# Performance work log

Measured on AMD Instinct MI355X. Metric: run time of the kernel, lower is better.

Reference implementation:

```python
import jax, jax.numpy as jnp
import numpy as np

C = 256
NH = 8
G = 32  # groupnorm groups (min(32, C))
EPS = 1e-6


def setup_inputs() -> dict:
    key = jax.random.key(0)
    ks = jax.random.split(key, 7)
    B, D, H, W = 2, 16, 16, 16
    x = jax.random.normal(ks[0], (B, C, D, H, W), dtype=jnp.float32)
    gn_gamma = jnp.ones((C,), jnp.float32)
    gn_beta = jnp.zeros((C,), jnp.float32)
    s = 1.0 / np.sqrt(C)
    qkv_w = jax.random.normal(ks[1], (3 * C, C), jnp.float32) * s  # 1x1x1 conv weight
    qkv_b = jnp.zeros((3 * C,), jnp.float32)
    proj_w = jax.random.normal(ks[2], (C, C), jnp.float32) * s
    proj_b = jnp.zeros((C,), jnp.float32)
    return {"x": x, "gn_gamma": gn_gamma, "gn_beta": gn_beta,
            "qkv_w": qkv_w, "qkv_b": qkv_b, "proj_w": proj_w, "proj_b": proj_b}


def _group_norm(x, gamma, beta):
    # x: [B, C, S]
    B, Cc, S = x.shape
    xg = x.reshape(B, G, (Cc // G) * S)
    mu = xg.mean(axis=-1, keepdims=True)
    var = xg.var(axis=-1, keepdims=True)
    xg = (xg - mu) * jax.lax.rsqrt(var + EPS)
    x = xg.reshape(B, Cc, S)
    return x * gamma[None, :, None] + beta[None, :, None]


def reference(x, gn_gamma, gn_beta, qkv_w, qkv_b, proj_w, proj_b):
    B, Cc, D, H, W = x.shape
    S = D * H * W
    hd = Cc // NH
    xf = x.reshape(B, Cc, S)
    h = _group_norm(xf, gn_gamma, gn_beta)
    # 1x1x1 conv == channel matmul: [B, 3C, S]
    qkv = jnp.einsum('oc,bcs->bos', qkv_w, h) + qkv_b[None, :, None]
    # torch path: reshape(B,3C,S).permute(0,2,1).chunk -> q=channels[0:C]
    q, k, v = qkv[:, :Cc], qkv[:, Cc:2 * Cc], qkv[:, 2 * Cc:]
    # [B, C, S] -> [B, NH, S, hd]
    def to_heads(t):
        return t.reshape(B, NH, hd, S).transpose(0, 1, 3, 2)
    q, k, v = to_heads(q), to_heads(k), to_heads(v)
    scale = hd ** (-0.5)
    attn = jax.nn.softmax(jnp.einsum('bnqd,bnkd->bnqk', q, k) * scale, axis=-1)
    o = jnp.einsum('bnqk,bnkd->bnqd', attn, v)  # [B, NH, S, hd]
    o = o.transpose(0, 1, 3, 2).reshape(B, Cc, S)  # back to [B, C, S]
    o = jnp.einsum('oc,bcs->bos', proj_w, o) + proj_b[None, :, None]
    return x + o.reshape(B, Cc, D, H, W)
```

## Files before the change

kernel.cpp:

```cpp
#include <hip/hip_runtime.h>
#include <cstddef>

#define S_LEN 4096
#define C_DIM 256
#define NHEADS 8
#define HDIM 32

typedef __attribute__((ext_vector_type(8))) _Float16 half8;
typedef __attribute__((ext_vector_type(4))) _Float16 half4;
typedef __attribute__((ext_vector_type(2))) _Float16 h2t;
typedef __attribute__((ext_vector_type(2))) __fp16 fp16x2;
typedef __attribute__((ext_vector_type(4))) float floatx4;

#define SC2F ((float)(0.17677669529663687 * 1.4426950408889634))

__global__ __launch_bounds__(256) void prep_stats(
    const float* __restrict__ qkv_w, const float* __restrict__ proj_w,
    const float* __restrict__ qkv_b, const float* __restrict__ x,
    _Float16* __restrict__ wq, _Float16* __restrict__ wp,
    float* __restrict__ qbias, float* __restrict__ gstat)
{
  const int blk = blockIdx.x;
  const int tid = threadIdx.x;
  if (blk < 64) {
    __shared__ float red[2][4];
    const int g = blk & 31, b = blk >> 5;
    const float* xb = x + ((size_t)b * C_DIM + g * 8) * S_LEN;
    const float4* x4 = (const float4*)xb;
    float sum = 0.f, sumsq = 0.f;
    for (int i = tid; i < 8192; i += 256) {
      float4 v = x4[i];
      sum += v.x + v.y + v.z + v.w;
      sumsq += v.x * v.x + v.y * v.y + v.z * v.z + v.w * v.w;
    }
    for (int off = 1; off < 64; off <<= 1) {
      sum += __shfl_xor(sum, off, 64);
      sumsq += __shfl_xor(sumsq, off, 64);
    }
    const int wv = tid >> 6, lane = tid & 63;
    if (lane == 0) { red[0][wv] = sum; red[1][wv] = sumsq; }
    __syncthreads();
    if (tid == 0) {
      float s = red[0][0] + red[0][1] + red[0][2] + red[0][3];
      float sq = red[1][0] + red[1][1] + red[1][2] + red[1][3];
      float mean = s * (1.f / 32768.f);
      float var = sq * (1.f / 32768.f) - mean * mean;
      gstat[((size_t)b * 32 + g) * 2 + 0] = mean;
      gstat[((size_t)b * 32 + g) * 2 + 1] = rsqrtf(var + 1e-6f);
    }
  } else {
    int idx = (blk - 64) * 256 + tid;
    if (idx < 768 * 256) {
      float v = qkv_w[idx];
      if (idx < 256 * 256) v *= SC2F;
      wq[idx] = (_Float16)v;
    } else if (idx < 768 * 256 + 256 * 256) {
      int i = idx - 768 * 256;
      wp[i] = (_Float16)proj_w[i];
    } else if (idx < 768 * 256 + 256 * 256 + 768) {
      int i = idx - (768 * 256 + 256 * 256);
      float bv = qkv_b[i];
      if (i < 256) bv *= SC2F;
      qbias[i] = bv;
    }
  }
}

__global__ __launch_bounds__(256) void qkv_gn_gemm(
    const _Float16* __restrict__ W, const float* __restrict__ bias,
    const float* __restrict__ x, const float* __restrict__ gamma,
    const float* __restrict__ beta, const float* __restrict__ gstat,
    _Float16* __restrict__ qo, _Float16* __restrict__ ko_,
    _Float16* __restrict__ vo)
{
  __shared__ __align__(16) _Float16 Ld[64 * 264];
  const int tid = threadIdx.x;
  const int b = blockIdx.z;
  const int s0 = blockIdx.y * 64;

  {
    const int c0 = (tid & 127) * 2, c1 = c0 + 1;
    const int sh = tid >> 7;
    const int g = c0 >> 3;
    const float mean = gstat[((size_t)b * 32 + g) * 2 + 0];
    const float rstd = gstat[((size_t)b * 32 + g) * 2 + 1];
    const float ga0 = gamma[c0] * rstd, be0 = beta[c0] - mean * ga0;
    const float ga1 = gamma[c1] * rstd, be1 = beta[c1] - mean * ga1;
    const float4* xa = (const float4*)(x + ((size_t)b * C_DIM + c0) * S_LEN + s0 + sh * 32);
    const float4* xc = (const float4*)(x + ((size_t)b * C_DIM + c1) * S_LEN + s0 + sh * 32);
    #pragma unroll
    for (int j = 0; j < 8; ++j) {
      float4 a = xa[j], c = xc[j];
      int sl = sh * 32 + j * 4;
      *(h2t*)&Ld[(sl + 0) * 264 + c0] = (h2t){ (_Float16)(a.x * ga0 + be0), (_Float16)(c.x * ga1 + be1) };
      *(h2t*)&Ld[(sl + 1) * 264 + c0] = (h2t){ (_Float16)(a.y * ga0 + be0), (_Float16)(c.y * ga1 + be1) };
      *(h2t*)&Ld[(sl + 2) * 264 + c0] = (h2t){ (_Float16)(a.z * ga0 + be0), (_Float16)(c.z * ga1 + be1) };
      *(h2t*)&Ld[(sl + 3) * 264 + c0] = (h2t){ (_Float16)(a.w * ga0 + be0), (_Float16)(c.w * ga1 + be1) };
    }
  }
  __syncthreads();

  const int lane = tid & 63, wv = tid >> 6;
  const int m = lane & 15, quad = lane >> 4;
  const int mtb = blockIdx.x * 8 + wv * 2;
  const _Float16* wrow0 = W + (size_t)((mtb + 0) * 16 + m) * C_DIM + quad * 8;
  const _Float16* wrow1 = W + (size_t)((mtb + 1) * 16 + m) * C_DIM + quad * 8;
  const _Float16* lp = &Ld[m * 264 + quad * 8];

  floatx4 acc[2][4];
  #pragma unroll
  for (int j = 0; j < 2; ++j)
    #pragma unroll
    for (int s = 0; s < 4; ++s) acc[j][s] = (floatx4){0.f,0.f,0.f,0.f};

  #pragma unroll
  for (int k0 = 0; k0 < C_DIM; k0 += 32) {
    half8 b0 = *(const half8*)(lp + k0);
    half8 b1 = *(const half8*)(lp + 16 * 264 + k0);
    half8 b2 = *(const half8*)(lp + 32 * 264 + k0);
    half8 b3 = *(const half8*)(lp + 48 * 264 + k0);
    half8 a0 = *(const half8*)(wrow0 + k0);
    half8 a1 = *(const half8*)(wrow1 + k0);
    acc[0][0] = __builtin_amdgcn_mfma_f32_16x16x32_f16(a0, b0, acc[0][0], 0, 0, 0);
    acc[0][1] = __builtin_amdgcn_mfma_f32_16x16x32_f16(a0, b1, acc[0][1], 0, 0, 0);
    acc[0][2] = __builtin_amdgcn_mfma_f32_16x16x32_f16(a0, b2, acc[0][2], 0, 0, 0);
    acc[0][3] = __builtin_amdgcn_mfma_f32_16x16x32_f16(a0, b3, acc[0][3], 0, 0, 0);
    acc[1][0] = __builtin_amdgcn_mfma_f32_16x16x32_f16(a1, b0, acc[1][0], 0, 0, 0);
    acc[1][1] = __builtin_amdgcn_mfma_f32_16x16x32_f16(a1, b1, acc[1][1], 0, 0, 0);
    acc[1][2] = __builtin_amdgcn_mfma_f32_16x16x32_f16(a1, b2, acc[1][2], 0, 0, 0);
    acc[1][3] = __builtin_amdgcn_mfma_f32_16x16x32_f16(a1, b3, acc[1][3], 0, 0, 0);
  }

  #pragma unroll
  for (int j = 0; j < 2; ++j) {
    const int ob = (mtb + j) * 16 + quad * 4;
    const float bv0 = bias[ob], bv1 = bias[ob + 1],
                bv2 = bias[ob + 2], bv3 = bias[ob + 3];
    #pragma unroll
    for (int sub = 0; sub < 4; ++sub) {
      int s = s0 + sub * 16 + m;
      float v0 = acc[j][sub][0] + bv0, v1 = acc[j][sub][1] + bv1,
            v2 = acc[j][sub][2] + bv2, v3 = acc[j][sub][3] + bv3;
      if (ob < 512) {
        _Float16* dst = (ob < 256) ? qo : ko_;
        int oo = ob & 255, n = oo >> 5, d0 = oo & 31;
        half4 h = { (_Float16)v0, (_Float16)v1, (_Float16)v2, (_Float16)v3 };
        *(half4*)(dst + (((size_t)b * NHEADS + n) * S_LEN + s) * HDIM + d0) = h;
      } else {
        int oo = ob - 512, n = oo >> 5, d0 = oo & 31;
        _Float16* dst = vo + ((size_t)b * NHEADS + n) * HDIM * S_LEN + s;
        dst[(size_t)(d0 + 0) * S_LEN] = (_Float16)v0;
        dst[(size_t)(d0 + 1) * S_LEN] = (_Float16)v1;
        dst[(size_t)(d0 + 2) * S_LEN] = (_Float16)v2;
        dst[(size_t)(d0 + 3) * S_LEN] = (_Float16)v3;
      }
    }
  }
}

__global__ __launch_bounds__(512) void attn_kernel(
    const _Float16* __restrict__ q, const _Float16* __restrict__ k,
    const _Float16* __restrict__ v, _Float16* __restrict__ po,
    float* __restrict__ pl)
{
  __shared__ __align__(16) _Float16 Kl[2][128 * 40];
  __shared__ __align__(16) _Float16 Vl[2][32 * 136];
  const int tid = threadIdx.x;
  const int lane = tid & 63, wv = tid >> 6;
  const int m = lane & 15, quad = lane >> 4;
  const int n = blockIdx.y, b = blockIdx.z;
  const int qc = blockIdx.x >> 1, kh = blockIdx.x & 1;
  const int q0 = qc * 128 + wv * 16;
  const int bh = b * NHEADS + n;

  const _Float16* qb = q + (size_t)bh * S_LEN * HDIM;
  const _Float16* kb = k + (size_t)bh * S_LEN * HDIM + (size_t)kh * 2048 * HDIM;
  const _Float16* vb = v + (size_t)bh * HDIM * S_LEN + (size_t)kh * 2048;

  half8 qf = *(const half8*)(qb + (size_t)(q0 + m) * HDIM + quad * 8);

  const int krow = tid >> 2, kc = (tid & 3) * 8;
  const int vrow = tid >> 4, vc = (tid & 15) * 8;
  const _Float16* kg = kb + (size_t)krow * HDIM + kc;
  const _Float16* vg = vb + (size_t)vrow * S_LEN + vc;
  const int klds = krow * 40 + kc;
  const int vlds = vrow * 136 + vc;

  int4 kreg = *(const int4*)kg;
  int4 vreg = *(const int4*)vg;
  const _Float16* kgp = kg + 128 * HDIM;
  const _Float16* vgp = vg + 128;

  floatx4 o0 = {0.f,0.f,0.f,0.f}, o1 = o0;
  float l0 = 0.f;
  const fp16x2 one2 = { (__fp16)1.0f, (__fp16)1.0f };

  #pragma unroll 2
  for (int it = 0; it < 16; ++it) {
    const int bufi = it & 1;
    *(int4*)(&Kl[bufi][klds]) = kreg;
    *(int4*)(&Vl[bufi][vlds]) = vreg;
    kreg = *(const int4*)kgp; kgp += 128 * HDIM;
    vreg = *(const int4*)vgp; vgp += 128;
    __syncthreads();
    const _Float16* Kb = Kl[bufi];
    const _Float16* Vb = Vl[bufi];
    #pragma unroll
    for (int t = 0; t < 8; ++t) {
      half8 kf = *(const half8*)(Kb + (t * 16 + m) * 40 + quad * 8);
      half4 vf0 = *(const half4*)(Vb + m * 136 + t * 16 + quad * 4);
      half4 vf1 = *(const half4*)(Vb + (16 + m) * 136 + t * 16 + quad * 4);
      floatx4 z = {0.f,0.f,0.f,0.f};
      floatx4 s0 = __builtin_amdgcn_mfma_f32_16x16x32_f16(kf, qf, z, 0, 0, 0);
      float e0 = __builtin_amdgcn_exp2f(s0[0]);
      float e1 = __builtin_amdgcn_exp2f(s0[1]);
      float e2 = __builtin_amdgcn_exp2f(s0[2]);
      float e3 = __builtin_amdgcn_exp2f(s0[3]);
      half4 p0;
      fp16x2 plo = __builtin_amdgcn_cvt_pkrtz(e0, e1);
      fp16x2 phi = __builtin_amdgcn_cvt_pkrtz(e2, e3);
      *(fp16x2*)&p0 = plo;
      *((fp16x2*)&p0 + 1) = phi;
      l0 = __builtin_amdgcn_fdot2(plo, one2, l0, false);
      l0 = __builtin_amdgcn_fdot2(phi, one2, l0, false);
      o0 = __builtin_amdgcn_mfma_f32_16x16x16f16(vf0, p0, o0, 0, 0, 0);
      o1 = __builtin_amdgcn_mfma_f32_16x16x16f16(vf1, p0, o1, 0, 0, 0);
    }
  }
  l0 += __shfl_xor(l0, 16, 64);
  l0 += __shfl_xor(l0, 32, 64);
  _Float16* poh = po + (size_t)kh * 2097152 + ((size_t)bh * S_LEN + q0 + m) * HDIM;
  half4 h0 = { (_Float16)o0[0], (_Float16)o0[1], (_Float16)o0[2], (_Float16)o0[3] };
  half4 h1 = { (_Float16)o1[0], (_Float16)o1[1], (_Float16)o1[2], (_Float16)o1[3] };
  *(half4*)(poh + quad * 4) = h0;
  *(half4*)(poh + 16 + quad * 4) = h1;
  if (quad == 0) pl[(size_t)kh * 65536 + (size_t)bh * S_LEN + q0 + m] = l0;
}

__global__ __launch_bounds__(256) void proj_gemm(
    const _Float16* __restrict__ W, const float* __restrict__ bias,
    const _Float16* __restrict__ po, const float* __restrict__ pl,
    const float* __restrict__ x, float* __restrict__ out)
{
  const int tid = threadIdx.x;
  const int lane = tid & 63, wv = tid >> 6;
  const int m = lane & 15, quad = lane >> 4;
  const int mt = blockIdx.x * 4 + wv;
  const int s0 = blockIdx.y * 64;
  const int b = blockIdx.z;
  const int row = mt * 16 + m;

  float inv[8][4];
  #pragma unroll
  for (int n = 0; n < 8; ++n) {
    #pragma unroll
    for (int sub = 0; sub < 4; ++sub) {
      size_t idx = ((size_t)(b * NHEADS + n)) * S_LEN + s0 + sub * 16 + m;
      inv[n][sub] = 1.f / (pl[idx] + pl[65536 + idx]);
    }
  }

  const _Float16* wrow = W + (size_t)row * C_DIM + quad * 8;
  floatx4 acc0 = {0.f,0.f,0.f,0.f}, acc1 = acc0, acc2 = acc0, acc3 = acc0;
  #pragma unroll
  for (int k0 = 0; k0 < C_DIM; k0 += 32) {
    const int n = k0 >> 5;
    const int d0 = quad * 8;
    half8 bf[4];
    #pragma unroll
    for (int sub = 0; sub < 4; ++sub) {
      size_t idx = (((size_t)(b * NHEADS + n)) * S_LEN + s0 + sub * 16 + m) * HDIM + d0;
      half8 a = *(const half8*)(po + idx);
      half8 c = *(const half8*)(po + 2097152 + idx);
      _Float16 iv = (_Float16)inv[n][sub];
      bf[sub] = (a + c) * iv;
    }
    half8 af = *(const half8*)(wrow + k0);
    acc0 = __builtin_amdgcn_mfma_f32_16x16x32_f16(af, bf[0], acc0, 0, 0, 0);
    acc1 = __builtin_amdgcn_mfma_f32_16x16x32_f16(af, bf[1], acc1, 0, 0, 0);
    acc2 = __builtin_amdgcn_mfma_f32_16x16x32_f16(af, bf[2], acc2, 0, 0, 0);
    acc3 = __builtin_amdgcn_mfma_f32_16x16x32_f16(af, bf[3], acc3, 0, 0, 0);
  }
  floatx4 accs[4] = {acc0, acc1, acc2, acc3};
  #pragma unroll
  for (int sub = 0; sub < 4; ++sub) {
    int s = s0 + sub * 16 + m;
    #pragma unroll
    for (int r = 0; r < 4; ++r) {
      int c = mt * 16 + quad * 4 + r;
      size_t idx = ((size_t)b * C_DIM + c) * S_LEN + s;
      out[idx] = x[idx] + accs[sub][r] + bias[c];
    }
  }
}

extern "C" void kernel_launch(void* const* d_in, const int* in_sizes, int n_in,
                              void* d_out, int out_size, void* d_ws, size_t ws_size,
                              hipStream_t stream) {
  const float* x        = (const float*)d_in[0];
  const float* gn_gamma = (const float*)d_in[1];
  const float* gn_beta  = (const float*)d_in[2];
  const float* qkv_w    = (const float*)d_in[3];
  const float* qkv_b    = (const float*)d_in[4];
  const float* proj_w   = (const float*)d_in[5];
  const float* proj_b   = (const float*)d_in[6];
  float* out = (float*)d_out;

  const size_t n1 = (size_t)2 * S_LEN * C_DIM;
  char* ws = (char*)d_ws;
  _Float16* qx  = (_Float16*)ws;
  _Float16* kx  = qx + n1;
  _Float16* vx  = kx + n1;
  _Float16* wq  = vx + n1;
  _Float16* wp  = wq + 768 * 256;
  float*    qbias = (float*)(wp + 256 * 256);
  float*    gstat = qbias + 768;
  _Float16* po  = (_Float16*)(gstat + 128);
  float*    pl  = (float*)(po + 2 * n1);

  prep_stats<<<1091, 256, 0, stream>>>(qkv_w, proj_w, qkv_b, x, wq, wp, qbias, gstat);
  qkv_gn_gemm<<<dim3(6, 64, 2), 256, 0, stream>>>(wq, qbias, x, gn_gamma, gn_beta, gstat, qx, kx, vx);
  attn_kernel<<<dim3(64, 8, 2), 512, 0, stream>>>(qx, kx, vx, po, pl);
  proj_gemm<<<dim3(4, 64, 2), 256, 0, stream>>>(wp, proj_b, po, pl, x, out);
}
```

Measured before the change: 171.1 us.

## Split keys across waves in attention, keep all queries in registers

Restructures the attention kernel so each of 4 waves holds all 128 query rows in registers and processes its own 32-key slice of each 128-key chunk. K and V fragments are loaded directly from global memory into registers, with no LDS staging and no per-iteration barrier. Partial outputs and row sums from the waves are reduced through LDS in a two-step tree at the end. This removes the LDS round-trip and the synchronization in the main loop, but greatly raises register pressure (16 accumulators plus 8 Q fragments) and halves the threads per block, which can lower occupancy. It also rounds the partial sums to fp16 during the cross-wave reduction.

```diff
diff --git a/kernel.cpp b/kernel.cpp
--- a/kernel.cpp
+++ b/kernel.cpp
@@ -158,83 +158,146 @@
   }
 }
 
-__global__ __launch_bounds__(512) void attn_kernel(
+__global__ __launch_bounds__(256) void attn_kernel(
     const _Float16* __restrict__ q, const _Float16* __restrict__ k,
     const _Float16* __restrict__ v, _Float16* __restrict__ po,
     float* __restrict__ pl)
 {
-  __shared__ __align__(16) _Float16 Kl[2][128 * 40];
-  __shared__ __align__(16) _Float16 Vl[2][32 * 136];
+  __shared__ unsigned int Ml[2][64][41];
   const int tid = threadIdx.x;
   const int lane = tid & 63, wv = tid >> 6;
   const int m = lane & 15, quad = lane >> 4;
   const int n = blockIdx.y, b = blockIdx.z;
   const int qc = blockIdx.x >> 1, kh = blockIdx.x & 1;
-  const int q0 = qc * 128 + wv * 16;
+  const int q0 = qc * 128;
   const int bh = b * NHEADS + n;
 
   const _Float16* qb = q + (size_t)bh * S_LEN * HDIM;
   const _Float16* kb = k + (size_t)bh * S_LEN * HDIM + (size_t)kh * 2048 * HDIM;
   const _Float16* vb = v + (size_t)bh * HDIM * S_LEN + (size_t)kh * 2048;
 
-  half8 qf = *(const half8*)(qb + (size_t)(q0 + m) * HDIM + quad * 8);
-
-  const int krow = tid >> 2, kc = (tid & 3) * 8;
-  const int vrow = tid >> 4, vc = (tid & 15) * 8;
-  const _Float16* kg = kb + (size_t)krow * HDIM + kc;
-  const _Float16* vg = vb + (size_t)vrow * S_LEN + vc;
-  const int klds = krow * 40 + kc;
-  const int vlds = vrow * 136 + vc;
-
-  int4 kreg = *(const int4*)kg;
-  int4 vreg = *(const int4*)vg;
-  const _Float16* kgp = kg + 128 * HDIM;
-  const _Float16* vgp = vg + 128;
-
-  floatx4 o0 = {0.f,0.f,0.f,0.f}, o1 = o0;
-  float l0 = 0.f;
+  half8 qf[8];
+  #pragma unroll
+  for (int j = 0; j < 8; ++j)
+    qf[j] = *(const half8*)(qb + (size_t)(q0 + j * 16 + m) * HDIM + quad * 8);
+
+  const _Float16* kp0 = kb + (size_t)(wv * 32 + m) * HDIM + quad * 8;
+  const _Float16* kp1 = kp0 + 16 * HDIM;
+  const _Float16* vp00 = vb + (size_t)m * S_LEN + wv * 32 + quad * 4;
+  const _Float16* vp01 = vp00 + 16;
+  const _Float16* vp10 = vp00 + (size_t)16 * S_LEN;
+  const _Float16* vp11 = vp10 + 16;
+
+  int4 kr0 = *(const int4*)kp0, kr1 = *(const int4*)kp1;
+  int2 v00 = *(const int2*)vp00, v01 = *(const int2*)vp01;
+  int2 v10 = *(const int2*)vp10, v11 = *(const int2*)vp11;
+
+  floatx4 o[8][2];
+  float l[8];
+  #pragma unroll
+  for (int j = 0; j < 8; ++j) {
+    o[j][0] = (floatx4){0.f,0.f,0.f,0.f};
+    o[j][1] = (floatx4){0.f,0.f,0.f,0.f};
+    l[j] = 0.f;
+  }
   const fp16x2 one2 = { (__fp16)1.0f, (__fp16)1.0f };
 
-  #pragma unroll 2
   for (int it = 0; it < 16; ++it) {
-    const int bufi = it & 1;
-    *(int4*)(&Kl[bufi][klds]) = kreg;
-    *(int4*)(&Vl[bufi][vlds]) = vreg;
-    kreg = *(const int4*)kgp; kgp += 128 * HDIM;
-    vreg = *(const int4*)vgp; vgp += 128;
-    __syncthreads();
-    const _Float16* Kb = Kl[bufi];
-    const _Float16* Vb = Vl[bufi];
-    #pragma unroll
-    for (int t = 0; t < 8; ++t) {
-      half8 kf = *(const half8*)(Kb + (t * 16 + m) * 40 + quad * 8);
-      half4 vf0 = *(const half4*)(Vb + m * 136 + t * 16 + quad * 4);
-      half4 vf1 = *(const half4*)(Vb + (16 + m) * 136 + t * 16 + quad * 4);
+    half8 kf0 = __builtin_bit_cast(half8, kr0);
+    half8 kf1 = __builtin_bit_cast(half8, kr1);
+    half4 vf00 = __builtin_bit_cast(half4, v00);
+    half4 vf01 = __builtin_bit_cast(half4, v01);
+    half4 vf10 = __builtin_bit_cast(half4, v10);
+    half4 vf11 = __builtin_bit_cast(half4, v11);
+    kp0 += 128 * HDIM; kp1 += 128 * HDIM;
+    vp00 += 128; vp01 += 128; vp10 += 128; vp11 += 128;
+    kr0 = *(const int4*)kp0; kr1 = *(const int4*)kp1;
+    v00 = *(const int2*)vp00; v01 = *(const int2*)vp01;
+    v10 = *(const int2*)vp10; v11 = *(const int2*)vp11;
+    #pragma unroll
+    for (int j = 0; j < 8; ++j) {
       floatx4 z = {0.f,0.f,0.f,0.f};
-      floatx4 s0 = __builtin_amdgcn_mfma_f32_16x16x32_f16(kf, qf, z, 0, 0, 0);
+      floatx4 s0 = __builtin_amdgcn_mfma_f32_16x16x32_f16(kf0, qf[j], z, 0, 0, 0);
+      floatx4 s1 = __builtin_amdgcn_mfma_f32_16x16x32_f16(kf1, qf[j], z, 0, 0, 0);
       float e0 = __builtin_amdgcn_exp2f(s0[0]);
       float e1 = __builtin_amdgcn_exp2f(s0[1]);
       float e2 = __builtin_amdgcn_exp2f(s0[2]);
       float e3 = __builtin_amdgcn_exp2f(s0[3]);
-      half4 p0;
-      fp16x2 plo = __builtin_amdgcn_cvt_pkrtz(e0, e1);
-      fp16x2 phi = __builtin_amdgcn_cvt_pkrtz(e2, e3);
-      *(fp16x2*)&p0 = plo;
-      *((fp16x2*)&p0 + 1) = phi;
-      l0 = __builtin_amdgcn_fdot2(plo, one2, l0, false);
-      l0 = __builtin_amdgcn_fdot2(phi, one2, l0, false);
-      o0 = __builtin_amdgcn_mfma_f32_16x16x16f16(vf0, p0, o0, 0, 0, 0);
-      o1 = __builtin_amdgcn_mfma_f32_16x16x16f16(vf1, p0, o1, 0, 0, 0);
-    }
-  }
-  l0 += __shfl_xor(l0, 16, 64);
-  l0 += __shfl_xor(l0, 32, 64);
-  _Float16* poh = po + (size_t)kh * 2097152 + ((size_t)bh * S_LEN + q0 + m) * HDIM;
-  half4 h0 = { (_Float16)o0[0], (_Float16)o0[1], (_Float16)o0[2], (_Float16)o0[3] };
-  half4 h1 = { (_Float16)o1[0], (_Float16)o1[1], (_Float16)o1[2], (_Float16)o1[3] };
-  *(half4*)(poh + quad * 4) = h0;
-  *(half4*)(poh + 16 + quad * 4) = h1;
-  if (quad == 0) pl[(size_t)kh * 65536 + (size_t)bh * S_LEN + q0 + m] = l0;
+      float f0 = __builtin_amdgcn_exp2f(s1[0]);
+      float f1 = __builtin_amdgcn_exp2f(s1[1]);
+      float f2 = __builtin_amdgcn_exp2f(s1[2]);
+      float f3 = __builtin_amdgcn_exp2f(s1[3]);
+      half4 p0, p1;
+      fp16x2 p0lo = __builtin_amdgcn_cvt_pkrtz(e0, e1);
+      fp16x2 p0hi = __builtin_amdgcn_cvt_pkrtz(e2, e3);
+      fp16x2 p1lo = __builtin_amdgcn_cvt_pkrtz(f0, f1);
+      fp16x2 p1hi = __builtin_amdgcn_cvt_pkrtz(f2, f3);
+      *(fp16x2*)&p0 = p0lo; *((fp16x2*)&p0 + 1) = p0hi;
+      *(fp16x2*)&p1 = p1lo; *((fp16x2*)&p1 + 1) = p1hi;
+      float lj = l[j];
+      lj = __builtin_amdgcn_fdot2(p0lo, one2, lj, false);
+      lj = __builtin_amdgcn_fdot2(p0hi, one2, lj, false);
+      lj = __builtin_amdgcn_fdot2(p1lo, one2, lj, false);
+      lj = __builtin_amdgcn_fdot2(p1hi, one2, lj, false);
+      l[j] = lj;
+      o[j][0] = __builtin_amdgcn_mfma_f32_16x16x16f16(vf00, p0, o[j][0], 0, 0, 0);
+      o[j][1] = __builtin_amdgcn_mfma_f32_16x16x16f16(vf10, p0, o[j][1], 0, 0, 0);
+      o[j][0] = __builtin_amdgcn_mfma_f32_16x16x16f16(vf01, p1, o[j][0], 0, 0, 0);
+      o[j][1] = __builtin_amdgcn_mfma_f32_16x16x16f16(vf11, p1, o[j][1], 0, 0, 0);
+    }
+  }
+
+  #define WRITE_SLOT(s)                                                      \
+    { unsigned int* d_ = &Ml[s][lane][0];                                    \
+      _Pragma("unroll") for (int j = 0; j < 8; ++j) {                        \
+        half4 h0_ = { (_Float16)o[j][0][0], (_Float16)o[j][0][1],            \
+                      (_Float16)o[j][0][2], (_Float16)o[j][0][3] };          \
+        half4 h1_ = { (_Float16)o[j][1][0], (_Float16)o[j][1][1],            \
+                      (_Float16)o[j][1][2], (_Float16)o[j][1][3] };          \
+        int2 a_ = __builtin_bit_cast(int2, h0_);                             \
+        int2 b_ = __builtin_bit_cast(int2, h1_);                             \
+        d_[j*4+0] = a_.x; d_[j*4+1] = a_.y;                                  \
+        d_[j*4+2] = b_.x; d_[j*4+3] = b_.y; }                                \
+      _Pragma("unroll") for (int j = 0; j < 8; ++j)                          \
+        d_[32+j] = __builtin_bit_cast(unsigned int, l[j]); }
+  #define ADD_SLOT(s)                                                        \
+    { const unsigned int* r_ = &Ml[s][lane][0];                              \
+      _Pragma("unroll") for (int j = 0; j < 8; ++j) {                        \
+        int2 a_ = { (int)r_[j*4+0], (int)r_[j*4+1] };                        \
+        int2 b_ = { (int)r_[j*4+2], (int)r_[j*4+3] };                        \
+        half4 h0_ = __builtin_bit_cast(half4, a_);                           \
+        half4 h1_ = __builtin_bit_cast(half4, b_);                           \
+        _Pragma("unroll") for (int r2 = 0; r2 < 4; ++r2) {                   \
+          o[j][0][r2] += (float)h0_[r2];                                     \
+          o[j][1][r2] += (float)h1_[r2]; } }                                 \
+      _Pragma("unroll") for (int j = 0; j < 8; ++j)                          \
+        l[j] += __builtin_bit_cast(float, r_[32+j]); }
+
+  if (wv >= 2) WRITE_SLOT(wv - 2);
+  __syncthreads();
+  if (wv < 2) ADD_SLOT(wv);
+  __syncthreads();
+  if (wv == 1) WRITE_SLOT(0);
+  __syncthreads();
+  if (wv == 0) {
+    ADD_SLOT(0);
+    _Float16* pob = po + (size_t)kh * 2097152 + ((size_t)bh * S_LEN) * HDIM;
+    #pragma unroll
+    for (int j = 0; j < 8; ++j) {
+      float lj = l[j];
+      lj += __shfl_xor(lj, 16, 64);
+      lj += __shfl_xor(lj, 32, 64);
+      int qrow = q0 + j * 16 + m;
+      half4 h0 = { (_Float16)o[j][0][0], (_Float16)o[j][0][1],
+                   (_Float16)o[j][0][2], (_Float16)o[j][0][3] };
+      half4 h1 = { (_Float16)o[j][1][0], (_Float16)o[j][1][1],
+                   (_Float16)o[j][1][2], (_Float16)o[j][1][3] };
+      _Float16* poh = pob + (size_t)qrow * HDIM;
+      *(half4*)(poh + quad * 4) = h0;
+      *(half4*)(poh + 16 + quad * 4) = h1;
+      if (quad == 0) pl[(size_t)kh * 65536 + (size_t)bh * S_LEN + qrow] = lj;
+    }
+  }
 }
 
 __global__ __launch_bounds__(256) void proj_gemm(
@@ -320,6 +383,6 @@
 
   prep_stats<<<1091, 256, 0, stream>>>(qkv_w, proj_w, qkv_b, x, wq, wp, qbias, gstat);
   qkv_gn_gemm<<<dim3(6, 64, 2), 256, 0, stream>>>(wq, qbias, x, gn_gamma, gn_beta, gstat, qx, kx, vx);
-  attn_kernel<<<dim3(64, 8, 2), 512, 0, stream>>>(qx, kx, vx, po, pl);
+  attn_kernel<<<dim3(64, 8, 2), 256, 0, stream>>>(qx, kx, vx, po, pl);
   proj_gemm<<<dim3(4, 64, 2), 256, 0, stream>>>(wp, proj_b, po, pl, x, out);
 }
```

New measurement: 191.4 us. 1.12x slower.

## Split groupnorm stats across more blocks and shrink attention K/V tiles

Applied to the files above, without the earlier changes.

The group-norm statistics pass is spread over 512 blocks that each write partial sums and sums of squares. The consuming GEMM kernel then reduces the 8 partials per group to get mean and rstd. This is meant to replace 64 long serial blocks with a wider, more parallel reduction. Separately, the attention kernel's K/V staging tile is halved from 128 to 64 keys, doubling loop iterations with smaller LDS buffers and 8-byte loads. That adds more barriers per key range in exchange for lower LDS use.

```diff
diff --git a/kernel.cpp b/kernel.cpp
--- a/kernel.cpp
+++ b/kernel.cpp
@@ -18,18 +18,20 @@
     const float* __restrict__ qkv_w, const float* __restrict__ proj_w,
     const float* __restrict__ qkv_b, const float* __restrict__ x,
     _Float16* __restrict__ wq, _Float16* __restrict__ wp,
-    float* __restrict__ qbias, float* __restrict__ gstat)
+    float* __restrict__ qbias, float* __restrict__ pstat)
 {
   const int blk = blockIdx.x;
   const int tid = threadIdx.x;
-  if (blk < 64) {
+  if (blk < 512) {
     __shared__ float red[2][4];
-    const int g = blk & 31, b = blk >> 5;
-    const float* xb = x + ((size_t)b * C_DIM + g * 8) * S_LEN;
+    const int gb = blk >> 3, e = blk & 7;
+    const int g = gb & 31, b = gb >> 5;
+    const float* xb = x + ((size_t)b * C_DIM + g * 8) * S_LEN + e * 4096;
     const float4* x4 = (const float4*)xb;
     float sum = 0.f, sumsq = 0.f;
-    for (int i = tid; i < 8192; i += 256) {
-      float4 v = x4[i];
+    #pragma unroll
+    for (int i = 0; i < 4; ++i) {
+      float4 v = x4[tid + i * 256];
       sum += v.x + v.y + v.z + v.w;
       sumsq += v.x * v.x + v.y * v.y + v.z * v.z + v.w * v.w;
     }
@@ -41,15 +43,11 @@
     if (lane == 0) { red[0][wv] = sum; red[1][wv] = sumsq; }
     __syncthreads();
     if (tid == 0) {
-      float s = red[0][0] + red[0][1] + red[0][2] + red[0][3];
-      float sq = red[1][0] + red[1][1] + red[1][2] + red[1][3];
-      float mean = s * (1.f / 32768.f);
-      float var = sq * (1.f / 32768.f) - mean * mean;
-      gstat[((size_t)b * 32 + g) * 2 + 0] = mean;
-      gstat[((size_t)b * 32 + g) * 2 + 1] = rsqrtf(var + 1e-6f);
+      pstat[(gb * 8 + e) * 2 + 0] = red[0][0] + red[0][1] + red[0][2] + red[0][3];
+      pstat[(gb * 8 + e) * 2 + 1] = red[1][0] + red[1][1] + red[1][2] + red[1][3];
     }
   } else {
-    int idx = (blk - 64) * 256 + tid;
+    int idx = (blk - 512) * 256 + tid;
     if (idx < 768 * 256) {
       float v = qkv_w[idx];
       if (idx < 256 * 256) v *= SC2F;
@@ -69,7 +67,7 @@
 __global__ __launch_bounds__(256) void qkv_gn_gemm(
     const _Float16* __restrict__ W, const float* __restrict__ bias,
     const float* __restrict__ x, const float* __restrict__ gamma,
-    const float* __restrict__ beta, const float* __restrict__ gstat,
+    const float* __restrict__ beta, const float* __restrict__ pstat,
     _Float16* __restrict__ qo, _Float16* __restrict__ ko_,
     _Float16* __restrict__ vo)
 {
@@ -82,8 +80,15 @@
     const int c0 = (tid & 127) * 2, c1 = c0 + 1;
     const int sh = tid >> 7;
     const int g = c0 >> 3;
-    const float mean = gstat[((size_t)b * 32 + g) * 2 + 0];
-    const float rstd = gstat[((size_t)b * 32 + g) * 2 + 1];
+    const int gb = b * 32 + g;
+    float s = 0.f, sq = 0.f;
+    #pragma unroll
+    for (int e = 0; e < 8; ++e) {
+      s  += pstat[(gb * 8 + e) * 2 + 0];
+      sq += pstat[(gb * 8 + e) * 2 + 1];
+    }
+    const float mean = s * (1.f / 32768.f);
+    const float rstd = rsqrtf(sq * (1.f / 32768.f) - mean * mean + 1e-6f);
     const float ga0 = gamma[c0] * rstd, be0 = beta[c0] - mean * ga0;
     const float ga1 = gamma[c1] * rstd, be1 = beta[c1] - mean * ga1;
     const float4* xa = (const float4*)(x + ((size_t)b * C_DIM + c0) * S_LEN + s0 + sh * 32);
@@ -163,8 +168,8 @@
     const _Float16* __restrict__ v, _Float16* __restrict__ po,
     float* __restrict__ pl)
 {
-  __shared__ __align__(16) _Float16 Kl[2][128 * 40];
-  __shared__ __align__(16) _Float16 Vl[2][32 * 136];
+  __shared__ __align__(16) _Float16 Kl[2][64 * 40];
+  __shared__ __align__(16) _Float16 Vl[2][32 * 68];
   const int tid = threadIdx.x;
   const int lane = tid & 63, wv = tid >> 6;
   const int m = lane & 15, quad = lane >> 4;
@@ -179,37 +184,37 @@
 
   half8 qf = *(const half8*)(qb + (size_t)(q0 + m) * HDIM + quad * 8);
 
-  const int krow = tid >> 2, kc = (tid & 3) * 8;
-  const int vrow = tid >> 4, vc = (tid & 15) * 8;
+  const int krow = wv * 8 + (lane >> 3), kc = (lane & 7) * 4;
+  const int vrow = wv * 4 + (lane >> 4), vc = (lane & 15) * 4;
   const _Float16* kg = kb + (size_t)krow * HDIM + kc;
   const _Float16* vg = vb + (size_t)vrow * S_LEN + vc;
   const int klds = krow * 40 + kc;
-  const int vlds = vrow * 136 + vc;
-
-  int4 kreg = *(const int4*)kg;
-  int4 vreg = *(const int4*)vg;
-  const _Float16* kgp = kg + 128 * HDIM;
-  const _Float16* vgp = vg + 128;
+  const int vlds = vrow * 68 + vc;
+
+  int2 kreg = *(const int2*)kg;
+  int2 vreg = *(const int2*)vg;
+  const _Float16* kgp = kg + 64 * HDIM;
+  const _Float16* vgp = vg + 64;
 
   floatx4 o0 = {0.f,0.f,0.f,0.f}, o1 = o0;
   float l0 = 0.f;
   const fp16x2 one2 = { (__fp16)1.0f, (__fp16)1.0f };
 
   #pragma unroll 2
-  for (int it = 0; it < 16; ++it) {
+  for (int it = 0; it < 32; ++it) {
     const int bufi = it & 1;
-    *(int4*)(&Kl[bufi][klds]) = kreg;
-    *(int4*)(&Vl[bufi][vlds]) = vreg;
-    kreg = *(const int4*)kgp; kgp += 128 * HDIM;
-    vreg = *(const int4*)vgp; vgp += 128;
+    *(int2*)(&Kl[bufi][klds]) = kreg;
+    *(int2*)(&Vl[bufi][vlds]) = vreg;
+    kreg = *(const int2*)kgp; kgp += 64 * HDIM;
+    vreg = *(const int2*)vgp; vgp += 64;
     __syncthreads();
     const _Float16* Kb = Kl[bufi];
     const _Float16* Vb = Vl[bufi];
     #pragma unroll
-    for (int t = 0; t < 8; ++t) {
+    for (int t = 0; t < 4; ++t) {
       half8 kf = *(const half8*)(Kb + (t * 16 + m) * 40 + quad * 8);
-      half4 vf0 = *(const half4*)(Vb + m * 136 + t * 16 + quad * 4);
-      half4 vf1 = *(const half4*)(Vb + (16 + m) * 136 + t * 16 + quad * 4);
+      half4 vf0 = *(const half4*)(Vb + m * 68 + t * 16 + quad * 4);
+      half4 vf1 = *(const half4*)(Vb + (16 + m) * 68 + t * 16 + quad * 4);
       floatx4 z = {0.f,0.f,0.f,0.f};
       floatx4 s0 = __builtin_amdgcn_mfma_f32_16x16x32_f16(kf, qf, z, 0, 0, 0);
       float e0 = __builtin_amdgcn_exp2f(s0[0]);
@@ -314,12 +319,12 @@
   _Float16* wq  = vx + n1;
   _Float16* wp  = wq + 768 * 256;
   float*    qbias = (float*)(wp + 256 * 256);
-  float*    gstat = qbias + 768;
-  _Float16* po  = (_Float16*)(gstat + 128);
+  float*    pstat = qbias + 768;
+  _Float16* po  = (_Float16*)(pstat + 1024);
   float*    pl  = (float*)(po + 2 * n1);
 
-  prep_stats<<<1091, 256, 0, stream>>>(qkv_w, proj_w, qkv_b, x, wq, wp, qbias, gstat);
-  qkv_gn_gemm<<<dim3(6, 64, 2), 256, 0, stream>>>(wq, qbias, x, gn_gamma, gn_beta, gstat, qx, kx, vx);
+  prep_stats<<<1539, 256, 0, stream>>>(qkv_w, proj_w, qkv_b, x, wq, wp, qbias, pstat);
+  qkv_gn_gemm<<<dim3(6, 64, 2), 256, 0, stream>>>(wq, qbias, x, gn_gamma, gn_beta, pstat, qx, kx, vx);
   attn_kernel<<<dim3(64, 8, 2), 512, 0, stream>>>(qx, kx, vx, po, pl);
   proj_gemm<<<dim3(4, 64, 2), 256, 0, stream>>>(wp, proj_b, po, pl, x, out);
 }
```

Result: faster. 156.2 us (-8.7%).
